# Optimization experiments

Hardware: AMD Instinct MI355X
Metric: run time of the kernel (lower is better)

## Reference

```python
import jax, jax.numpy as jnp
import numpy as np
import math

DIM = 1024
N_HEAD = 16
HEAD_DIM = DIM // N_HEAD  # 64
B, T = 4, 2048


def rotate_half(x):
    # lucidrains-style interleaved rotation: (x1, x2) pairs -> (-x2, x1)
    x = x.reshape(*x.shape[:-1], -1, 2)
    x1, x2 = x[..., 0], x[..., 1]
    return jnp.stack((-x2, x1), axis=-1).reshape(*x.shape[:-2], -1)


def apply_rope(x):
    # x: [b, h, t, d]
    d = x.shape[-1]
    t = x.shape[-2]
    inv_freq = 1.0 / (10000.0 ** (jnp.arange(0, d, 2, dtype=jnp.float32) / d))  # [d/2]
    angles = jnp.arange(t, dtype=jnp.float32)[:, None] * inv_freq[None, :]      # [t, d/2]
    angles = jnp.repeat(angles, 2, axis=-1)                                     # [t, d] interleaved
    cos, sin = jnp.cos(angles), jnp.sin(angles)
    return x * cos + rotate_half(x) * sin


def setup_inputs() -> dict:
    key = jax.random.key(0)
    kx, kw1, kb1, kw2, kb2 = jax.random.split(key, 5)
    x = jax.random.normal(kx, (B, T, DIM), dtype=jnp.float32)
    mask = jnp.tril(jnp.ones((T, T), dtype=jnp.int32))  # causal
    s = 0.02
    qkv_w = jax.random.normal(kw1, (DIM, 3 * DIM), dtype=jnp.float32) * s
    qkv_b = jax.random.normal(kb1, (3 * DIM,), dtype=jnp.float32) * s
    out_w = jax.random.normal(kw2, (DIM, DIM), dtype=jnp.float32) * s
    out_b = jax.random.normal(kb2, (DIM,), dtype=jnp.float32) * s
    return {"x": x, "mask": mask, "qkv_w": qkv_w, "qkv_b": qkv_b,
            "out_w": out_w, "out_b": out_b}


def reference(x, mask, qkv_w, qkv_b, out_w, out_b):
    b, t, _ = x.shape
    qkv = x @ qkv_w + qkv_b                       # [b, t, 3*dim]
    q, k, v = jnp.split(qkv, 3, axis=-1)
    def to_heads(z):
        return z.reshape(b, t, N_HEAD, HEAD_DIM).transpose(0, 2, 1, 3)  # [b,h,t,d]
    q, k, v = to_heads(q), to_heads(k), to_heads(v)
    q = apply_rope(q)
    k = apply_rope(k)
    scores = jnp.einsum('bhqd,bhkd->bhqk', q, k) / math.sqrt(HEAD_DIM)
    scores = jnp.where(mask[None, None, :, :] == 0, -jnp.inf, scores)
    attn = jax.nn.softmax(scores, axis=-1)        # dropout = identity (eval)
    out = jnp.einsum('bhqk,bhkd->bhqd', attn, v)  # [b,h,t,d]
    out = out.transpose(0, 2, 1, 3).reshape(b, t, DIM)
    return out @ out_w + out_b
```

## Files before the change

### kernel.cpp

```cpp
#include <hip/hip_runtime.h>

typedef __bf16 bf16_t;
typedef __bf16 bf16x8 __attribute__((ext_vector_type(8)));
typedef float  f32x4  __attribute__((ext_vector_type(4)));
typedef float  f32x16 __attribute__((ext_vector_type(16)));
typedef unsigned u32x4 __attribute__((ext_vector_type(4)));

#define DIMM  1024
#define NHEAD 16
#define HDIM  64
#define BATCH 4
#define SEQ   2048
#define MROWS (BATCH*SEQ)

#define AQB   128
#define AKV   64
#define NP    (SEQ/AQB)
#define SKS   72
#define LOG2E 1.44269504088896f

__device__ __forceinline__ void gload_lds16(const bf16_t* g, bf16_t* l) {
  __builtin_amdgcn_global_load_lds(
      (const __attribute__((address_space(1))) void*)g,
      (__attribute__((address_space(3))) void*)l, 16, 0, 0);
}

__device__ __forceinline__ unsigned short f2bu(float f) {
  bf16_t b = (bf16_t)f;
  return __builtin_bit_cast(unsigned short, b);
}
__device__ __forceinline__ float bu2f(unsigned short u) {
  return __uint_as_float(((unsigned)u) << 16);
}
__device__ __forceinline__ unsigned packbf(float a, float b) {
  return (unsigned)f2bu(a) | ((unsigned)f2bu(b) << 16);
}
__device__ __forceinline__ float fexp2(float x) {
  float r; asm("v_exp_f32 %0, %1" : "=v"(r) : "v"(x)); return r;
}

__global__ void k_convert(const float* __restrict__ in, bf16_t* __restrict__ out, int n4) {
  int i = blockIdx.x * blockDim.x + threadIdx.x;
  if (i >= n4) return;
  float4 v = reinterpret_cast<const float4*>(in)[i];
  ushort4 o;
  o.x = f2bu(v.x); o.y = f2bu(v.y); o.z = f2bu(v.z); o.w = f2bu(v.w);
  reinterpret_cast<ushort4*>(out)[i] = o;
}

__global__ void k_transpose_convert(const float* __restrict__ in, bf16_t* __restrict__ out,
                                    int R, int C) {
  __shared__ float tile[32][33];
  int cb = blockIdx.x * 32, rb = blockIdx.y * 32;
  int tx = threadIdx.x, ty = threadIdx.y;
  #pragma unroll
  for (int i = 0; i < 4; ++i)
    tile[ty + i*8][tx] = in[(size_t)(rb + ty + i*8) * C + cb + tx];
  __syncthreads();
  #pragma unroll
  for (int i = 0; i < 4; ++i)
    out[(size_t)(cb + ty + i*8) * R + rb + tx] = (bf16_t)tile[tx][ty + i*8];
}

__global__ void k_rope_table(float* __restrict__ cosT, float* __restrict__ sinT) {
  int id = blockIdx.x * blockDim.x + threadIdx.x;
  if (id >= SEQ * 32) return;
  int t = id >> 5, i = id & 31;
  double ang = (double)t * pow(10000.0, -(double)i / 32.0);
  cosT[id] = (float)cos(ang);
  sinT[id] = (float)sin(ang);
}

__global__ void k_rope(bf16_t* __restrict__ Q, bf16_t* __restrict__ Kb,
                       const float* __restrict__ cosT, const float* __restrict__ sinT) {
  int id = blockIdx.x * blockDim.x + threadIdx.x;
  if (id >= 64 * SEQ * 32) return;
  int i = id & 31;
  int t = (id >> 5) & (SEQ - 1);
  float c = cosT[(t << 5) + i], s = sinT[(t << 5) + i];
  unsigned* Qu = reinterpret_cast<unsigned*>(Q);
  unsigned* Ku = reinterpret_cast<unsigned*>(Kb);
  const float qs = 0.125f * LOG2E;
  {
    unsigned u = Qu[id];
    float x1 = bu2f((unsigned short)(u & 0xffffu));
    float x2 = bu2f((unsigned short)(u >> 16));
    Qu[id] = packbf((x1 * c - x2 * s) * qs, (x2 * c + x1 * s) * qs);
  }
  {
    unsigned u = Ku[id];
    float x1 = bu2f((unsigned short)(u & 0xffffu));
    float x2 = bu2f((unsigned short)(u >> 16));
    Ku[id] = packbf(x1 * c - x2 * s, x2 * c + x1 * s);
  }
}

__global__ __launch_bounds__(512, 2) void k_gemm0(
    const bf16_t* __restrict__ A, const bf16_t* __restrict__ BT,
    const float* __restrict__ bias,
    bf16_t* __restrict__ q, bf16_t* __restrict__ k, bf16_t* __restrict__ v)
{
  __shared__ bf16_t sA[2][2][128 * 64];
  __shared__ bf16_t sB[2][2][128 * 64];

  const int tid = threadIdx.x;
  const int w = tid >> 6;
  const int lane = tid & 63;
  const int wm = w >> 2, wn = w & 3;
  const int l15 = lane & 15, l4 = lane >> 4;

  int nwg = gridDim.x * gridDim.y;
  int id  = blockIdx.y * gridDim.x + blockIdx.x;
  int cpx = nwg >> 3;
  int sid = (id & 7) * cpx + (id >> 3);
  int bx = sid % gridDim.x, by = sid / gridDim.x;
  const int rowA0 = by * 256, colB0 = bx * 256;

  f32x4 acc[8][4] = {};
  bf16x8 bf_[4];

  auto stage = [&](int tile, int part) {
    if (tile >= 16) return;
    const int kh = part >> 1;
    const bool isB = part & 1;
    const bf16_t* src = isB ? BT : A;
    const int r0 = isB ? colB0 : rowA0;
    bf16_t* dst = (isB ? &sB[0][0][0] : &sA[0][0][0]) + ((tile & 1) * 2 + kh) * (128 * 64);
    #pragma unroll
    for (int call = 0; call < 2; ++call) {
      int n = call * 512 + tid;
      int R = n >> 3, slot = n & 7;
      int sp = slot ^ (R & 7);
      int row = R * 2 + (sp >> 2);
      gload_lds16(src + (size_t)(r0 + row) * 1024 + tile * 64 + kh * 32 + (sp & 3) * 8,
                  dst + n * 8);
    }
  };

  auto rdA = [&](int bc, int kh, int mfa) -> bf16x8 {
    int row = wm * 128 + mfa * 16 + l15;
    int R = row >> 1;
    int slot = (((row & 1) << 2) | l4) ^ (R & 7);
    return *reinterpret_cast<const bf16x8*>(&sA[bc][kh][R * 64 + slot * 8]);
  };
  auto rdB = [&](int bc, int kh, int nf) -> bf16x8 {
    int row = wn * 64 + nf * 16 + l15;
    int R = row >> 1;
    int slot = (((row & 1) << 2) | l4) ^ (R & 7);
    return *reinterpret_cast<const bf16x8*>(&sB[bc][kh][R * 64 + slot * 8]);
  };

  auto phase = [&](int bc, int kh, int mh, int stile, int spart, int wait_n) {
    bf16x8 af[4];
    if (mh == 0) {
      #pragma unroll
      for (int nf = 0; nf < 4; ++nf) bf_[nf] = rdB(bc, kh, nf);
    }
    #pragma unroll
    for (int mf = 0; mf < 4; ++mf) af[mf] = rdA(bc, kh, mh * 4 + mf);
    stage(stile, spart);
    if (wait_n == 4)      asm volatile("s_waitcnt vmcnt(4)" ::: "memory");
    else if (wait_n == 0) asm volatile("s_waitcnt vmcnt(0)" ::: "memory");
    __builtin_amdgcn_s_barrier();
    __builtin_amdgcn_s_setprio(1);
    #pragma unroll
    for (int mf = 0; mf < 4; ++mf)
      #pragma unroll
      for (int nf = 0; nf < 4; ++nf)
        acc[mh * 4 + mf][nf] = __builtin_amdgcn_mfma_f32_16x16x32_bf16(
            af[mf], bf_[nf], acc[mh * 4 + mf][nf], 0, 0, 0);
    __builtin_amdgcn_s_setprio(0);
    __builtin_amdgcn_s_barrier();
  };

  stage(0, 0); stage(0, 1); stage(0, 2); stage(0, 3);
  stage(1, 0); stage(1, 1);
  asm volatile("s_waitcnt vmcnt(4)" ::: "memory");
  __builtin_amdgcn_s_barrier();

  for (int i = 0; i < 8; ++i) {
    const int t0 = 2 * i, t1 = 2 * i + 1;
    phase(0, 0, 0, t1,     2, -1);
    phase(0, 0, 1, t1,     3, -1);
    phase(0, 1, 0, t0 + 2, 0, -1);
    phase(0, 1, 1, t0 + 2, 1, (t0 + 2 < 16) ? 4 : 0);
    phase(1, 0, 0, t0 + 2, 2, -1);
    phase(1, 0, 1, t0 + 2, 3, -1);
    phase(1, 1, 0, t0 + 3, 0, -1);
    phase(1, 1, 1, t0 + 3, 1, (t0 + 3 < 16) ? 4 : 0);
  }

  #pragma unroll
  for (int mfa = 0; mfa < 8; ++mfa) {
    #pragma unroll
    for (int nf = 0; nf < 4; ++nf) {
      int n = colB0 + wn * 64 + nf * 16 + l15;
      float bs = bias[n];
      int which = n >> 10, hd = n & 1023;
      int h = hd >> 6, d = hd & 63;
      bf16_t* dst = (which == 0) ? q : (which == 1) ? k : v;
      #pragma unroll
      for (int r = 0; r < 4; ++r) {
        int m = rowA0 + wm * 128 + mfa * 16 + l4 * 4 + r;
        int b = m >> 11, t = m & 2047;
        dst[((size_t)(b * NHEAD + h) * SEQ + t) * HDIM + d] = (bf16_t)(acc[mfa][nf][r] + bs);
      }
    }
  }
}

__global__ __launch_bounds__(256) void k_gemm1(
    const bf16_t* __restrict__ A, const bf16_t* __restrict__ BT,
    const float* __restrict__ bias, float* __restrict__ outf, int M, int N, int K)
{
  __shared__ bf16_t sA[128 * 32];
  __shared__ bf16_t sB[128 * 32];
  const int tid = threadIdx.x;
  const int w = tid >> 6, lane = tid & 63;
  const int wr = w >> 1, wc = w & 1;
  const int l15 = lane & 15, l4 = lane >> 4;

  int nwg = gridDim.x * gridDim.y;
  int id  = blockIdx.y * gridDim.x + blockIdx.x;
  int cpx = nwg >> 3;
  int sid = (id & 7) * cpx + (id >> 3);
  int bx = sid % gridDim.x, by = sid / gridDim.x;

  const int rowA0 = by * 128;
  const int colB0 = bx * 128;

  f32x4 acc[4][4] = {};

  const int nkt = K >> 5;
  for (int kt = 0; kt < nkt; ++kt) {
    __syncthreads();
    #pragma unroll
    for (int i = 0; i < 2; ++i) {
      int c = i * 256 + w * 64 + lane;
      int row = c >> 2, k8 = (c & 3) * 8;
      gload_lds16(A  + (size_t)(rowA0 + row) * K + kt * 32 + k8, sA + (i * 256 + w * 64) * 8);
      gload_lds16(BT + (size_t)(colB0 + row) * K + kt * 32 + k8, sB + (i * 256 + w * 64) * 8);
    }
    asm volatile("s_waitcnt vmcnt(0)" ::: "memory");
    __syncthreads();
    bf16x8 af[4], bfr[4];
    #pragma unroll
    for (int mi = 0; mi < 4; ++mi)
      af[mi] = *reinterpret_cast<const bf16x8*>(sA + (wr * 64 + mi * 16 + l15) * 32 + l4 * 8);
    #pragma unroll
    for (int ni = 0; ni < 4; ++ni)
      bfr[ni] = *reinterpret_cast<const bf16x8*>(sB + (wc * 64 + ni * 16 + l15) * 32 + l4 * 8);
    #pragma unroll
    for (int mi = 0; mi < 4; ++mi)
      #pragma unroll
      for (int ni = 0; ni < 4; ++ni)
        acc[mi][ni] = __builtin_amdgcn_mfma_f32_16x16x32_bf16(af[mi], bfr[ni], acc[mi][ni], 0, 0, 0);
  }

  #pragma unroll
  for (int mi = 0; mi < 4; ++mi) {
    #pragma unroll
    for (int ni = 0; ni < 4; ++ni) {
      int n = colB0 + wc * 64 + ni * 16 + l15;
      float bs = bias[n];
      #pragma unroll
      for (int r = 0; r < 4; ++r) {
        int m = rowA0 + wr * 64 + mi * 16 + l4 * 4 + r;
        outf[(size_t)m * N + n] = acc[mi][ni][r] + bs;
      }
    }
  }
}

__global__ __launch_bounds__(256, 2) void k_attn(
    const bf16_t* __restrict__ Q, const bf16_t* __restrict__ Kb,
    const bf16_t* __restrict__ Vb, bf16_t* __restrict__ O)
{
  __shared__ bf16_t sK[2][64 * SKS];
  __shared__ bf16_t sV[2][64 * SKS];

  const int tid = threadIdx.x;
  const int w = tid >> 6, lane = tid & 63;
  const int l31 = lane & 31, hi = lane >> 5;

  const int id = blockIdx.x;
  const int j4 = id >> 8;
  const int k4 = (id >> 6) & 3;
  const int bh = id & 63;
  const int qblk = (j4 == 0) ? 15 - 2 * k4
                 : (j4 == 1) ? 2 * k4
                 : (j4 == 2) ? 14 - 2 * k4
                 :             2 * k4 + 1;

  const size_t hbase = (size_t)bh * SEQ * HDIM;
  const int b = bh >> 4, h = bh & 15;
  const int srow = tid >> 3, sslot = tid & 7;

  const int qbase = qblk * AQB + 32 * w;
  const int nt = 2 * qblk + 2;

  bf16x8 qf[4];
  #pragma unroll
  for (int kt = 0; kt < 4; ++kt)
    qf[kt] = *reinterpret_cast<const bf16x8*>(
        Q + hbase + (size_t)(qbase + l31) * HDIM + kt * 16 + hi * 8);
  asm volatile("s_waitcnt vmcnt(0)" ::: "memory");
  asm volatile("" : "+v"(qf[0]), "+v"(qf[1]), "+v"(qf[2]), "+v"(qf[3]));

  u32x4 kr[2], vr[2];
  auto issue = [&](int t) {
    const bf16_t* kp = Kb + hbase + (size_t)(t * AKV + srow) * HDIM + sslot * 8;
    const bf16_t* vp = Vb + hbase + (size_t)(t * AKV + srow) * HDIM + sslot * 8;
    asm volatile("global_load_dwordx4 %0, %1, off" : "=v"(kr[0]) : "v"(kp));
    asm volatile("global_load_dwordx4 %0, %1, off" : "=v"(kr[1]) : "v"(kp + 32 * HDIM));
    asm volatile("global_load_dwordx4 %0, %1, off" : "=v"(vr[0]) : "v"(vp));
    asm volatile("global_load_dwordx4 %0, %1, off" : "=v"(vr[1]) : "v"(vp + 32 * HDIM));
  };
  auto stage = [&](int nb) {
    #pragma unroll
    for (int cc = 0; cc < 2; ++cc) {
      int row = srow + 32 * cc;
      *reinterpret_cast<u32x4*>(&sK[nb][row * SKS + ((sslot ^ (row >> 3)) << 3)]) = kr[cc];
      bf16x8 vv = __builtin_bit_cast(bf16x8, vr[cc]);
      #pragma unroll
      for (int j = 0; j < 8; ++j) {
        int d = sslot * 8 + j;
        sV[nb][d * SKS + (((row >> 3) ^ sslot) << 3) + (row & 7)] = vv[j];
      }
    }
  };

  float mrun = -1e30f, lrun = 0.f;
  f32x16 accO[2] = {};

  issue(0);
  asm volatile("s_waitcnt vmcnt(0)" ::: "memory");
  stage(0);
  issue(1);
  asm volatile("s_waitcnt lgkmcnt(0)" ::: "memory");
  __builtin_amdgcn_s_barrier();
  asm volatile("" ::: "memory");

  for (int t = 0; t < nt; ++t) {
    const int c = t & 1;
    if (t + 1 < nt) {
      asm volatile("s_waitcnt vmcnt(0)" ::: "memory");
      stage(c ^ 1);
      if (t + 2 < nt) issue(t + 2);
    }
    const bool masked = (t * AKV + AKV - 1 > qbase);
    #pragma unroll
    for (int sub = 0; sub < 2; ++sub) {
      f32x16 sc = {};
      __builtin_amdgcn_s_setprio(1);
      #pragma unroll
      for (int kt = 0; kt < 4; ++kt) {
        int krow = 32 * sub + l31;
        bf16x8 kf = *reinterpret_cast<const bf16x8*>(
            &sK[c][krow * SKS + (((2 * kt + hi) ^ (krow >> 3)) << 3)]);
        sc = __builtin_amdgcn_mfma_f32_32x32x16_bf16(kf, qf[kt], sc, 0, 0, 0);
      }
      __builtin_amdgcn_s_setprio(0);

      float p[16];
      const int qa = qbase + l31;
      const int kb0 = t * AKV + 32 * sub + 4 * hi;
      #pragma unroll
      for (int r = 0; r < 16; ++r) {
        float s = sc[r];
        if (masked) {
          int kvi = kb0 + (r & 3) + 8 * (r >> 2);
          if (kvi > qa) s = -1e30f;
        }
        p[r] = s;
      }
      float m0 = fmaxf(fmaxf(p[0],  p[1]),  p[2]);
      float m1 = fmaxf(fmaxf(p[3],  p[4]),  p[5]);
      float m2 = fmaxf(fmaxf(p[6],  p[7]),  p[8]);
      float m3 = fmaxf(fmaxf(p[9],  p[10]), p[11]);
      float m4 = fmaxf(fmaxf(p[12], p[13]), p[14]);
      float mt = fmaxf(fmaxf(fmaxf(m0, m1), fmaxf(m2, m3)), fmaxf(m4, p[15]));
      mt = fmaxf(mt, __shfl_xor(mt, 32));
      if (!__all(mt <= mrun + 11.54f)) {
        float mnew = fmaxf(mrun, mt);
        float scl = fexp2(mrun - mnew);
        mrun = mnew;
        lrun *= scl;
        #pragma unroll
        for (int i = 0; i < 16; ++i) { accO[0][i] *= scl; accO[1][i] *= scl; }
      }
      float rs = 0.f;
      #pragma unroll
      for (int r = 0; r < 16; ++r) { p[r] = fexp2(p[r] - mrun); rs += p[r]; }
      lrun += rs + __shfl_xor(rs, 32);

      bf16x8 pf[2];
      #pragma unroll
      for (int kt = 0; kt < 2; ++kt) {
        unsigned P01 = packbf(p[8*kt+0], p[8*kt+1]);
        unsigned P23 = packbf(p[8*kt+2], p[8*kt+3]);
        unsigned P45 = packbf(p[8*kt+4], p[8*kt+5]);
        unsigned P67 = packbf(p[8*kt+6], p[8*kt+7]);
        unsigned ra = __shfl_xor(hi == 0 ? P45 : P01, 32);
        unsigned rb = __shfl_xor(hi == 0 ? P67 : P23, 32);
        unsigned dw0 = hi == 0 ? P01 : ra;
        unsigned dw1 = hi == 0 ? P23 : rb;
        unsigned dw2 = hi == 0 ? ra : P45;
        unsigned dw3 = hi == 0 ? rb : P67;
        pf[kt] = __builtin_bit_cast(bf16x8, (u32x4){dw0, dw1, dw2, dw3});
      }

      __builtin_amdgcn_s_setprio(1);
      #pragma unroll
      for (int dt = 0; dt < 2; ++dt) {
        #pragma unroll
        for (int kt = 0; kt < 2; ++kt) {
          int vrow = 32 * dt + l31;
          bf16x8 vf = *reinterpret_cast<const bf16x8*>(
              &sV[c][vrow * SKS + (((4 * sub + 2 * kt + hi) ^ (vrow >> 3)) << 3)]);
          accO[dt] = __builtin_amdgcn_mfma_f32_32x32x16_bf16(vf, pf[kt], accO[dt], 0, 0, 0);
        }
      }
      __builtin_amdgcn_s_setprio(0);
    }
    asm volatile("s_waitcnt lgkmcnt(0)" ::: "memory");
    __builtin_amdgcn_s_barrier();
    asm volatile("" ::: "memory");
  }

  bf16_t* sOw = &sK[0][0] + w * (32 * SKS);
  float inv = 1.f / lrun;
  #pragma unroll
  for (int dt = 0; dt < 2; ++dt)
    #pragma unroll
    for (int r = 0; r < 16; ++r) {
      int d = 32 * dt + (r & 3) + 8 * (r >> 2) + 4 * hi;
      sOw[l31 * SKS + (d ^ ((l31 >> 3) << 3))] = (bf16_t)(accO[dt][r] * inv);
    }
  #pragma unroll
  for (int i = 0; i < 4; ++i) {
    int qr = 8 * i + (lane >> 3);
    int ch = lane & 7;
    bf16x8 vvv = *reinterpret_cast<const bf16x8*>(
        &sOw[qr * SKS + ((ch ^ (qr >> 3)) << 3)]);
    *reinterpret_cast<bf16x8*>(
        O + ((size_t)(b * SEQ + qbase + qr)) * DIMM + h * HDIM + ch * 8) = vvv;
  }
}

extern "C" void kernel_launch(void* const* d_in, const int* in_sizes, int n_in,
                              void* d_out, int out_size, void* d_ws, size_t ws_size,
                              hipStream_t stream) {
  const float* x     = (const float*)d_in[0];
  const float* qkv_w = (const float*)d_in[2];
  const float* qkv_b = (const float*)d_in[3];
  const float* out_w = (const float*)d_in[4];
  const float* out_b = (const float*)d_in[5];
  float* out = (float*)d_out;

  char* ws = (char*)d_ws;
  size_t off = 0;
  auto alloc = [&](size_t bytes) {
    char* p = ws + off;
    off += (bytes + 255) & ~(size_t)255;
    return (void*)p;
  };
  bf16_t* Xb    = (bf16_t*)alloc((size_t)MROWS * DIMM * 2);
  bf16_t* WqkvT = (bf16_t*)alloc((size_t)3 * DIMM * DIMM * 2);
  bf16_t* WoutT = (bf16_t*)alloc((size_t)DIMM * DIMM * 2);
  bf16_t* Qh    = (bf16_t*)alloc((size_t)64 * SEQ * HDIM * 2);
  bf16_t* Kh    = (bf16_t*)alloc((size_t)64 * SEQ * HDIM * 2);
  bf16_t* Vh    = (bf16_t*)alloc((size_t)64 * SEQ * HDIM * 2);
  bf16_t* AO    = (bf16_t*)alloc((size_t)MROWS * DIMM * 2);
  float*  cosT  = (float*)alloc((size_t)SEQ * 32 * 4);
  float*  sinT  = (float*)alloc((size_t)SEQ * 32 * 4);

  k_convert<<<(MROWS * DIMM / 4 + 255) / 256, 256, 0, stream>>>(x, Xb, MROWS * DIMM / 4);
  k_transpose_convert<<<dim3(3 * DIMM / 32, DIMM / 32), dim3(32, 8), 0, stream>>>(qkv_w, WqkvT, DIMM, 3 * DIMM);
  k_transpose_convert<<<dim3(DIMM / 32, DIMM / 32), dim3(32, 8), 0, stream>>>(out_w, WoutT, DIMM, DIMM);
  k_rope_table<<<(SEQ * 32 + 255) / 256, 256, 0, stream>>>(cosT, sinT);

  k_gemm0<<<dim3(3 * DIMM / 256, MROWS / 256), 512, 0, stream>>>(
      Xb, WqkvT, qkv_b, Qh, Kh, Vh);

  k_rope<<<(64 * SEQ * 32 + 255) / 256, 256, 0, stream>>>(Qh, Kh, cosT, sinT);

  k_attn<<<dim3(NP * 64), 256, 0, stream>>>(Qh, Kh, Vh, AO);

  k_gemm1<<<dim3(DIMM / 128, MROWS / 128), 256, 0, stream>>>(
      AO, WoutT, out_b, out, MROWS, DIMM, DIMM);
}
```

Before: 203.6 us.

## Fuse RoPE into QKV GEMM epilogue and emit V pre-transposed

The separate RoPE kernel is removed. Rotation and the Q scale are now applied in the QKV GEMM epilogue, using a lane shuffle to fetch the paired element and reading cos/sin from the table. V is written transposed ([bh, d, t]) with 4-wide packed stores, so the attention kernel can stage V into LDS with a single vector store instead of eight scalar scattered writes. This removes a full read/write pass over Q and K and cuts LDS store work in attention. In exchange the epilogue does per-element table loads and shuffles, and the transposed V stores are strided across sequence.

```diff
diff --git a/kernel.cpp b/kernel.cpp
--- a/kernel.cpp
+++ b/kernel.cpp
@@ -71,34 +71,11 @@
   sinT[id] = (float)sin(ang);
 }
 
-__global__ void k_rope(bf16_t* __restrict__ Q, bf16_t* __restrict__ Kb,
-                       const float* __restrict__ cosT, const float* __restrict__ sinT) {
-  int id = blockIdx.x * blockDim.x + threadIdx.x;
-  if (id >= 64 * SEQ * 32) return;
-  int i = id & 31;
-  int t = (id >> 5) & (SEQ - 1);
-  float c = cosT[(t << 5) + i], s = sinT[(t << 5) + i];
-  unsigned* Qu = reinterpret_cast<unsigned*>(Q);
-  unsigned* Ku = reinterpret_cast<unsigned*>(Kb);
-  const float qs = 0.125f * LOG2E;
-  {
-    unsigned u = Qu[id];
-    float x1 = bu2f((unsigned short)(u & 0xffffu));
-    float x2 = bu2f((unsigned short)(u >> 16));
-    Qu[id] = packbf((x1 * c - x2 * s) * qs, (x2 * c + x1 * s) * qs);
-  }
-  {
-    unsigned u = Ku[id];
-    float x1 = bu2f((unsigned short)(u & 0xffffu));
-    float x2 = bu2f((unsigned short)(u >> 16));
-    Ku[id] = packbf(x1 * c - x2 * s, x2 * c + x1 * s);
-  }
-}
-
 __global__ __launch_bounds__(512, 2) void k_gemm0(
     const bf16_t* __restrict__ A, const bf16_t* __restrict__ BT,
     const float* __restrict__ bias,
-    bf16_t* __restrict__ q, bf16_t* __restrict__ k, bf16_t* __restrict__ v)
+    bf16_t* __restrict__ q, bf16_t* __restrict__ k, bf16_t* __restrict__ vt,
+    const float* __restrict__ cosT, const float* __restrict__ sinT)
 {
   __shared__ bf16_t sA[2][2][128 * 64];
   __shared__ bf16_t sB[2][2][128 * 64];
@@ -190,20 +167,49 @@
     phase(1, 1, 1, t0 + 3, 1, (t0 + 3 < 16) ? 4 : 0);
   }
 
-  #pragma unroll
-  for (int mfa = 0; mfa < 8; ++mfa) {
-    #pragma unroll
-    for (int nf = 0; nf < 4; ++nf) {
-      int n = colB0 + wn * 64 + nf * 16 + l15;
-      float bs = bias[n];
-      int which = n >> 10, hd = n & 1023;
-      int h = hd >> 6, d = hd & 63;
-      bf16_t* dst = (which == 0) ? q : (which == 1) ? k : v;
-      #pragma unroll
-      for (int r = 0; r < 4; ++r) {
-        int m = rowA0 + wm * 128 + mfa * 16 + l4 * 4 + r;
-        int b = m >> 11, t = m & 2047;
-        dst[((size_t)(b * NHEAD + h) * SEQ + t) * HDIM + d] = (bf16_t)(acc[mfa][nf][r] + bs);
+  const bool isV = (bx >= 8);
+  const bool isQ = (bx < 4);
+  const float qs = 0.125f * LOG2E;
+  if (isV) {
+    #pragma unroll
+    for (int mfa = 0; mfa < 8; ++mfa) {
+      #pragma unroll
+      for (int nf = 0; nf < 4; ++nf) {
+        int n = colB0 + wn * 64 + nf * 16 + l15;
+        int h = (n >> 6) & 15, d = n & 63;
+        float bs = bias[n];
+        int m0 = rowA0 + wm * 128 + mfa * 16 + l4 * 4;
+        int b = m0 >> 11, t = m0 & 2047;
+        ushort4 pk;
+        pk.x = f2bu(acc[mfa][nf][0] + bs);
+        pk.y = f2bu(acc[mfa][nf][1] + bs);
+        pk.z = f2bu(acc[mfa][nf][2] + bs);
+        pk.w = f2bu(acc[mfa][nf][3] + bs);
+        *reinterpret_cast<ushort4*>(
+            vt + ((size_t)((b * NHEAD + h) * HDIM + d)) * SEQ + t) = pk;
+      }
+    }
+  } else {
+    bf16_t* dst = isQ ? q : k;
+    #pragma unroll
+    for (int mfa = 0; mfa < 8; ++mfa) {
+      #pragma unroll
+      for (int nf = 0; nf < 4; ++nf) {
+        int n = colB0 + wn * 64 + nf * 16 + l15;
+        int h = (n >> 6) & 15, d = n & 63;
+        int i2 = d >> 1;
+        float bs = bias[n];
+        #pragma unroll
+        for (int r = 0; r < 4; ++r) {
+          int m = rowA0 + wm * 128 + mfa * 16 + l4 * 4 + r;
+          int b = m >> 11, t = m & 2047;
+          float val = acc[mfa][nf][r] + bs;
+          float prt = __shfl_xor(val, 1);
+          float c = cosT[(t << 5) + i2], s = sinT[(t << 5) + i2];
+          float y = (d & 1) ? (val * c + prt * s) : (val * c - prt * s);
+          if (isQ) y *= qs;
+          dst[((size_t)(b * NHEAD + h) * SEQ + t) * HDIM + d] = (bf16_t)y;
+        }
       }
     }
   }
@@ -274,7 +280,7 @@
 
 __global__ __launch_bounds__(256, 2) void k_attn(
     const bf16_t* __restrict__ Q, const bf16_t* __restrict__ Kb,
-    const bf16_t* __restrict__ Vb, bf16_t* __restrict__ O)
+    const bf16_t* __restrict__ Vt, bf16_t* __restrict__ O)
 {
   __shared__ bf16_t sK[2][64 * SKS];
   __shared__ bf16_t sV[2][64 * SKS];
@@ -310,23 +316,18 @@
   u32x4 kr[2], vr[2];
   auto issue = [&](int t) {
     const bf16_t* kp = Kb + hbase + (size_t)(t * AKV + srow) * HDIM + sslot * 8;
-    const bf16_t* vp = Vb + hbase + (size_t)(t * AKV + srow) * HDIM + sslot * 8;
+    const bf16_t* vp = Vt + hbase + (size_t)srow * SEQ + t * AKV + sslot * 8;
     asm volatile("global_load_dwordx4 %0, %1, off" : "=v"(kr[0]) : "v"(kp));
     asm volatile("global_load_dwordx4 %0, %1, off" : "=v"(kr[1]) : "v"(kp + 32 * HDIM));
     asm volatile("global_load_dwordx4 %0, %1, off" : "=v"(vr[0]) : "v"(vp));
-    asm volatile("global_load_dwordx4 %0, %1, off" : "=v"(vr[1]) : "v"(vp + 32 * HDIM));
+    asm volatile("global_load_dwordx4 %0, %1, off" : "=v"(vr[1]) : "v"(vp + 32 * SEQ));
   };
   auto stage = [&](int nb) {
     #pragma unroll
     for (int cc = 0; cc < 2; ++cc) {
       int row = srow + 32 * cc;
       *reinterpret_cast<u32x4*>(&sK[nb][row * SKS + ((sslot ^ (row >> 3)) << 3)]) = kr[cc];
-      bf16x8 vv = __builtin_bit_cast(bf16x8, vr[cc]);
-      #pragma unroll
-      for (int j = 0; j < 8; ++j) {
-        int d = sslot * 8 + j;
-        sV[nb][d * SKS + (((row >> 3) ^ sslot) << 3) + (row & 7)] = vv[j];
-      }
+      *reinterpret_cast<u32x4*>(&sV[nb][row * SKS + ((sslot ^ (row >> 3)) << 3)]) = vr[cc];
     }
   };
 
@@ -470,7 +471,7 @@
   bf16_t* WoutT = (bf16_t*)alloc((size_t)DIMM * DIMM * 2);
   bf16_t* Qh    = (bf16_t*)alloc((size_t)64 * SEQ * HDIM * 2);
   bf16_t* Kh    = (bf16_t*)alloc((size_t)64 * SEQ * HDIM * 2);
-  bf16_t* Vh    = (bf16_t*)alloc((size_t)64 * SEQ * HDIM * 2);
+  bf16_t* Vth   = (bf16_t*)alloc((size_t)64 * HDIM * SEQ * 2);
   bf16_t* AO    = (bf16_t*)alloc((size_t)MROWS * DIMM * 2);
   float*  cosT  = (float*)alloc((size_t)SEQ * 32 * 4);
   float*  sinT  = (float*)alloc((size_t)SEQ * 32 * 4);
@@ -481,11 +482,9 @@
   k_rope_table<<<(SEQ * 32 + 255) / 256, 256, 0, stream>>>(cosT, sinT);
 
   k_gemm0<<<dim3(3 * DIMM / 256, MROWS / 256), 512, 0, stream>>>(
-      Xb, WqkvT, qkv_b, Qh, Kh, Vh);
-
-  k_rope<<<(64 * SEQ * 32 + 255) / 256, 256, 0, stream>>>(Qh, Kh, cosT, sinT);
-
-  k_attn<<<dim3(NP * 64), 256, 0, stream>>>(Qh, Kh, Vh, AO);
+      Xb, WqkvT, qkv_b, Qh, Kh, Vth, cosT, sinT);
+
+  k_attn<<<dim3(NP * 64), 256, 0, stream>>>(Qh, Kh, Vth, AO);
 
   k_gemm1<<<dim3(DIMM / 128, MROWS / 128), 256, 0, stream>>>(
       AO, WoutT, out_b, out, MROWS, DIMM, DIMM);
```

Measured after the change: 195.6 us. 4.0% less time.
